# Kernel optimization log

Hardware: AMD Instinct MI355X
Metric: run time of the kernel (lower is better)

## Reference

```python
import jax, jax.numpy as jnp
import numpy as np
from jax import lax

NUM_DISP = 64
BLOCK = 21
EPS = 1e-12  # F.normalize default eps


def _box_sum(v):
    # v: (N, H, W) -> BLOCK x BLOCK zero-padded box sum (same shape), separable.
    p = BLOCK // 2
    v = v[:, None]  # (N,1,H,W)
    kv = jnp.ones((1, 1, BLOCK, 1), v.dtype)
    kh = jnp.ones((1, 1, 1, BLOCK), v.dtype)
    v = lax.conv_general_dilated(v, kv, (1, 1), ((p, p), (0, 0)))
    v = lax.conv_general_dilated(v, kh, (1, 1), ((0, 0), (p, p)))
    return v[:, 0]


def _l2norm_c(img):
    n = jnp.sqrt(jnp.sum(img * img, axis=1, keepdims=True))
    return img / jnp.maximum(n, EPS)


def _disparity(left, right):
    # left, right: (B, 3, H, W)
    left = _l2norm_c(left)
    right = _l2norm_c(right)
    B, C, H, W = left.shape
    d = jnp.arange(NUM_DISP)
    xs = jnp.arange(W)
    idx = xs[None, :] - d[:, None]              # (D, W): source column in right image
    valid = (idx >= 0)
    r_shift = right[:, :, :, jnp.clip(idx, 0)]  # (B, C, H, D, W)
    r_shift = jnp.where(valid[None, None, None], r_shift, 0.0)
    # per-pixel channel-summed absolute difference -> (B, D, H, W)
    diff = jnp.sum(jnp.abs(left[:, :, :, None, :] - r_shift), axis=1)  # (B, H, D, W)
    diff = jnp.transpose(diff, (0, 2, 1, 3))    # (B, D, H, W)
    cost = _box_sum(diff.reshape(B * NUM_DISP, H, W)).reshape(B, NUM_DISP, H, W)
    cost = cost / (C * BLOCK * BLOCK)           # mean SAD over block elements
    return jnp.argmin(cost, axis=1).astype(left.dtype)  # (B, H, W)


def setup_inputs() -> dict:
    key = jax.random.key(0)
    k1, k2 = jax.random.split(key)
    x = jax.random.normal(k1, (2, 6, 320, 512), dtype=jnp.float32)
    gt = jax.random.normal(k2, (2, 6, 320, 512), dtype=jnp.float32)
    return {"x": x, "gt": gt}


def reference(x, gt):
    disp_gt = _disparity(gt[:, :3], gt[:, 3:])
    disp_pred = _disparity(x[:, :3], x[:, 3:])
    return jnp.mean(jnp.abs(disp_pred - disp_gt))
```

## Files before the change

kernel.cpp:

```cpp
#include <hip/hip_runtime.h>
#include <math.h>

constexpr int B = 2, H = 320, W = 512, D = 64;
constexpr int HW = H * W;
constexpr int R = 10;
constexpr int SEG = 80;
constexpr int NSEG = H / SEG;
constexpr float EPS = 1e-12f;
constexpr int PADW = W + 2 * R;

__global__ void k_norm(const float* __restrict__ x, const float* __restrict__ gt,
                       float4* __restrict__ nrm4) {
    int idx = blockIdx.x * blockDim.x + threadIdx.x;
    if (idx >= 2 * B * HW) return;
    int t = idx / (B * HW);
    int rem = idx - t * (B * HW);
    int b = rem / HW;
    int hw = rem - b * HW;
    const float* p = (t == 0 ? x : gt) + (size_t)b * 6 * HW + hw;
    float v0 = p[0],      v1 = p[HW],     v2 = p[2 * HW];
    float v3 = p[3 * HW], v4 = p[4 * HW], v5 = p[5 * HW];
    float n1 = fmaxf(sqrtf(v0 * v0 + v1 * v1 + v2 * v2), EPS);
    float n2 = fmaxf(sqrtf(v3 * v3 + v4 * v4 + v5 * v5), EPS);
    float4* q = nrm4 + (size_t)(t * B + b) * 2 * HW + hw;
    q[0]  = make_float4(v0 / n1, v1 / n1, v2 / n1, 0.f);
    q[HW] = make_float4(v3 / n2, v4 / n2, v5 / n2, 0.f);
}

__global__ void k_cost(const float4* __restrict__ nrm4, float* __restrict__ cost, int t) {
    int blk = blockIdx.x;
    int combo = blk & (2 * NSEG - 1);
    int d = blk >> 3;
    int b = combo >> 2;
    int seg = combo & (NSEG - 1);
    int w = threadIdx.x;
    const float4* L4 = nrm4 + (size_t)(t * B + b) * 2 * HW;
    const float4* R4 = L4 + HW;
    const bool val = (w >= d);
    const int wr = val ? (w - d) : 0;
    const int h0 = seg * SEG;

    __shared__ float srow[2][PADW];
    if (w < R) {
        srow[0][w] = 0.f; srow[1][w] = 0.f;
        srow[0][W + R + w] = 0.f; srow[1][W + R + w] = 0.f;
    }

    auto diff = [&](int h) -> float {
        float4 l = L4[(size_t)h * W + w];
        if (val) {
            float4 r = R4[(size_t)h * W + wr];
            return fabsf(l.x - r.x) + fabsf(l.y - r.y) + fabsf(l.z - r.z);
        }
        return fabsf(l.x) + fabsf(l.y) + fabsf(l.z);
    };

    float ring[2 * R + 1];
    float s = 0.f;
#pragma unroll
    for (int j = 0; j < 2 * R + 1; ++j) {
        int hh = h0 - R + j;
        float v = (hh >= 0 && hh < H) ? diff(hh) : 0.f;
        ring[j] = v;
        s += v;
    }

    float* cp = cost + ((size_t)(b * D + d) * H) * W + w;
    for (int i = 0; i < SEG; ++i) {
        int h = h0 + i;
        float* row = srow[i & 1];
        row[R + w] = s;
        __syncthreads();
        float c = 0.f;
#pragma unroll
        for (int k = 0; k <= 2 * R; ++k) c += row[w + k];
        cp[(size_t)h * W] = c;
        int ha = h + R + 1;
        float nv = (ha < H) ? diff(ha) : 0.f;
        s += nv - ring[0];
#pragma unroll
        for (int j = 0; j < 2 * R; ++j) ring[j] = ring[j + 1];
        ring[2 * R] = nv;
    }
}

__global__ void k_argmin(const float* __restrict__ cost, float* __restrict__ disp) {
    int idx = blockIdx.x * blockDim.x + threadIdx.x;
    if (idx >= B * HW) return;
    int b = idx / HW;
    int hw = idx - b * HW;
    const float* cp = cost + (size_t)b * D * HW + hw;
    float best = 3.4e38f;
    int bd = 0;
    for (int d = 0; d < D; ++d) {
        float v = cp[(size_t)d * HW];
        if (v < best) { best = v; bd = d; }
    }
    disp[idx] = (float)bd;
}

__global__ void k_red1(const float* __restrict__ a, const float* __restrict__ b2,
                       float* __restrict__ part, int n) {
    __shared__ float sm[256];
    int tid = threadIdx.x;
    float s = 0.f;
    for (int i = blockIdx.x * 256 + tid; i < n; i += gridDim.x * 256)
        s += fabsf(a[i] - b2[i]);
    sm[tid] = s;
    __syncthreads();
    for (int off = 128; off; off >>= 1) {
        if (tid < off) sm[tid] += sm[tid + off];
        __syncthreads();
    }
    if (!tid) part[blockIdx.x] = sm[0];
}

__global__ void k_red2(const float* __restrict__ part, float* __restrict__ out,
                       int nb, float inv) {
    __shared__ float sm[256];
    int tid = threadIdx.x;
    float s = 0.f;
    for (int i = tid; i < nb; i += 256) s += part[i];
    sm[tid] = s;
    __syncthreads();
    for (int off = 128; off; off >>= 1) {
        if (tid < off) sm[tid] += sm[tid + off];
        __syncthreads();
    }
    if (!tid) out[0] = sm[0] * inv;
}

extern "C" void kernel_launch(void* const* d_in, const int* in_sizes, int n_in,
                              void* d_out, int out_size, void* d_ws, size_t ws_size,
                              hipStream_t stream) {
    const float* x  = (const float*)d_in[0];
    const float* gt = (const float*)d_in[1];

    float4* nrm4 = (float4*)d_ws;
    float* cost  = (float*)(nrm4 + (size_t)2 * B * 2 * HW);
    float* disp  = cost + (size_t)B * D * HW;
    float* part  = disp + (size_t)2 * B * HW;

    k_norm<<<(2 * B * HW + 255) / 256, 256, 0, stream>>>(x, gt, nrm4);

    for (int t = 0; t < 2; ++t) {
        k_cost<<<B * NSEG * D, W, 0, stream>>>(nrm4, cost, t);
        k_argmin<<<(B * HW + 255) / 256, 256, 0, stream>>>(cost, disp + (size_t)t * B * HW);
    }

    constexpr int NB = 640;
    k_red1<<<NB, 256, 0, stream>>>(disp, disp + (size_t)B * HW, part, B * HW);
    k_red2<<<1, 256, 0, stream>>>(part, (float*)d_out, NB, 1.f / (float)(B * HW));
}
```

Baseline: 241.5 us.

## Batch eight rows per barrier in cost kernel with shared ring and vectorized sliding sums

The cost kernel moves the vertical ring buffer into shared memory and accumulates eight rows of vertical sums before each barrier. Each thread then computes eight horizontal box sums with a running sliding window and writes them as float4 stores. This replaces the per-row barrier and 21 shared reads per output. The argmin kernel now processes four pixels per thread with float4 loads. In exchange the kernel uses more shared memory (about 60 KB per block), which may limit occupancy, and it adds a launch bound.

```diff
diff --git a/kernel.cpp b/kernel.cpp
--- a/kernel.cpp
+++ b/kernel.cpp
@@ -6,8 +6,8 @@
 constexpr int R = 10;
 constexpr int SEG = 80;
 constexpr int NSEG = H / SEG;
+constexpr int RS = 540;
 constexpr float EPS = 1e-12f;
-constexpr int PADW = W + 2 * R;
 
 __global__ void k_norm(const float* __restrict__ x, const float* __restrict__ gt,
                        float4* __restrict__ nrm4) {
@@ -27,12 +27,13 @@
     q[HW] = make_float4(v3 / n2, v4 / n2, v5 / n2, 0.f);
 }
 
-__global__ void k_cost(const float4* __restrict__ nrm4, float* __restrict__ cost, int t) {
+__global__ __launch_bounds__(512, 4) void k_cost(const float4* __restrict__ nrm4,
+                                                 float* __restrict__ cost, int t) {
     int blk = blockIdx.x;
-    int combo = blk & (2 * NSEG - 1);
+    int combo = blk & 7;
     int d = blk >> 3;
     int b = combo >> 2;
-    int seg = combo & (NSEG - 1);
+    int seg = combo & 3;
     int w = threadIdx.x;
     const float4* L4 = nrm4 + (size_t)(t * B + b) * 2 * HW;
     const float4* R4 = L4 + HW;
@@ -40,10 +41,13 @@
     const int wr = val ? (w - d) : 0;
     const int h0 = seg * SEG;
 
-    __shared__ float srow[2][PADW];
-    if (w < R) {
-        srow[0][w] = 0.f; srow[1][w] = 0.f;
-        srow[0][W + R + w] = 0.f; srow[1][W + R + w] = 0.f;
+    __shared__ float ring[21][W];
+    __shared__ float vsbuf[8][RS];
+
+    {
+        int j = w >> 6, k = w & 63;
+        if (k < 10) vsbuf[j][k] = 0.f;
+        else if (k < 28) vsbuf[j][522 + (k - 10)] = 0.f;
     }
 
     auto diff = [&](int h) -> float {
@@ -55,48 +59,74 @@
         return fabsf(l.x) + fabsf(l.y) + fabsf(l.z);
     };
 
-    float ring[2 * R + 1];
-    float s = 0.f;
+    float vs = 0.f;
+    for (int k = 0; k < 20; ++k) {
+        int h = h0 - R + k;
+        float dv = (h >= 0) ? diff(h) : 0.f;
+        ring[k][w] = dv;
+        vs += dv;
+    }
+    ring[20][w] = 0.f;
+
+    float* cp = cost + ((size_t)(b * D + d) * H) * W;
+    const int cc = threadIdx.x >> 3;
+    const int jj = threadIdx.x & 7;
+
+    for (int ss = 0; ss < SEG / 8; ++ss) {
 #pragma unroll
-    for (int j = 0; j < 2 * R + 1; ++j) {
-        int hh = h0 - R + j;
-        float v = (hh >= 0 && hh < H) ? diff(hh) : 0.f;
-        ring[j] = v;
-        s += v;
-    }
-
-    float* cp = cost + ((size_t)(b * D + d) * H) * W + w;
-    for (int i = 0; i < SEG; ++i) {
-        int h = h0 + i;
-        float* row = srow[i & 1];
-        row[R + w] = s;
+        for (int j = 0; j < 8; ++j) {
+            int i = ss * 8 + j;
+            int slot = (i + 20) % 21;
+            int hn = h0 + i + R;
+            float dv = (hn < H) ? diff(hn) : 0.f;
+            float dold = ring[slot][w];
+            ring[slot][w] = dv;
+            vs += dv - dold;
+            vsbuf[j][10 + w] = vs;
+        }
         __syncthreads();
-        float c = 0.f;
+        {
+            const float* vp = &vsbuf[jj][8 * cc];
+            float wnd[28];
 #pragma unroll
-        for (int k = 0; k <= 2 * R; ++k) c += row[w + k];
-        cp[(size_t)h * W] = c;
-        int ha = h + R + 1;
-        float nv = (ha < H) ? diff(ha) : 0.f;
-        s += nv - ring[0];
+            for (int q = 0; q < 7; ++q) {
+                float4 v4 = *(const float4*)(vp + 4 * q);
+                wnd[4 * q] = v4.x; wnd[4 * q + 1] = v4.y;
+                wnd[4 * q + 2] = v4.z; wnd[4 * q + 3] = v4.w;
+            }
+            float o = 0.f;
 #pragma unroll
-        for (int j = 0; j < 2 * R; ++j) ring[j] = ring[j + 1];
-        ring[2 * R] = nv;
+            for (int k = 0; k < 21; ++k) o += wnd[k];
+            float out[8];
+            out[0] = o;
+#pragma unroll
+            for (int k = 1; k < 8; ++k) { o += wnd[20 + k] - wnd[k - 1]; out[k] = o; }
+            float* op = cp + (size_t)(h0 + ss * 8 + jj) * W + 8 * cc;
+            *(float4*)(op)     = make_float4(out[0], out[1], out[2], out[3]);
+            *(float4*)(op + 4) = make_float4(out[4], out[5], out[6], out[7]);
+        }
+        __syncthreads();
     }
 }
 
 __global__ void k_argmin(const float* __restrict__ cost, float* __restrict__ disp) {
-    int idx = blockIdx.x * blockDim.x + threadIdx.x;
-    if (idx >= B * HW) return;
-    int b = idx / HW;
-    int hw = idx - b * HW;
-    const float* cp = cost + (size_t)b * D * HW + hw;
-    float best = 3.4e38f;
-    int bd = 0;
-    for (int d = 0; d < D; ++d) {
-        float v = cp[(size_t)d * HW];
-        if (v < best) { best = v; bd = d; }
+    int idx = blockIdx.x * 256 + threadIdx.x;
+    if (idx >= B * (HW / 4)) return;
+    int b = idx / (HW / 4);
+    int g = idx - b * (HW / 4);
+    const float4* cp = (const float4*)cost + (size_t)b * D * (HW / 4) + g;
+    float4 v0 = cp[0];
+    float bb[4] = {v0.x, v0.y, v0.z, v0.w};
+    int bd[4] = {0, 0, 0, 0};
+#pragma unroll 4
+    for (int d = 1; d < D; ++d) {
+        float4 v = cp[(size_t)d * (HW / 4)];
+        if (v.x < bb[0]) { bb[0] = v.x; bd[0] = d; }
+        if (v.y < bb[1]) { bb[1] = v.y; bd[1] = d; }
+        if (v.z < bb[2]) { bb[2] = v.z; bd[2] = d; }
+        if (v.w < bb[3]) { bb[3] = v.w; bd[3] = d; }
     }
-    disp[idx] = (float)bd;
+    ((float4*)disp)[idx] = make_float4((float)bd[0], (float)bd[1], (float)bd[2], (float)bd[3]);
 }
 
 __global__ void k_red1(const float* __restrict__ a, const float* __restrict__ b2,
@@ -144,8 +174,8 @@
     k_norm<<<(2 * B * HW + 255) / 256, 256, 0, stream>>>(x, gt, nrm4);
 
     for (int t = 0; t < 2; ++t) {
-        k_cost<<<B * NSEG * D, W, 0, stream>>>(nrm4, cost, t);
-        k_argmin<<<(B * HW + 255) / 256, 256, 0, stream>>>(cost, disp + (size_t)t * B * HW);
+        k_cost<<<B * NSEG * D, 512, 0, stream>>>(nrm4, cost, t);
+        k_argmin<<<(B * (HW / 4) + 255) / 256, 256, 0, stream>>>(cost, disp + (size_t)t * B * HW);
     }
 
     constexpr int NB = 640;
```

After: 203.9 us. 1.18x faster.

## Split box filter into vertical-sum pass and fused horizontal-sum argmin kernel

Applied to the files above, without the earlier changes.

The cost kernel now only computes vertical running sums and writes them to a zero-padded row buffer, with no shared memory and no per-row barrier. A new kernel reads those padded rows, applies the horizontal 21-wide sliding sum in registers, and takes the argmin over disparities in the same pass, so the full cost volume is never written and re-read. The second image's pass also folds the absolute-difference loss and a per-block reduction into the argmin kernel, removing the separate reduction kernel. In exchange the vertical-sum buffer is padded and slightly larger, and the normalisation runs per image instead of once for both.

```diff
diff --git a/kernel.cpp b/kernel.cpp
--- a/kernel.cpp
+++ b/kernel.cpp
@@ -4,115 +4,144 @@
 constexpr int B = 2, H = 320, W = 512, D = 64;
 constexpr int HW = H * W;
 constexpr int R = 10;
-constexpr int SEG = 80;
-constexpr int NSEG = H / SEG;
+constexpr int SEG = 80, NSEG = 4;
+constexpr int VS = 536;
 constexpr float EPS = 1e-12f;
-constexpr int PADW = W + 2 * R;
 
-__global__ void k_norm(const float* __restrict__ x, const float* __restrict__ gt,
-                       float4* __restrict__ nrm4) {
-    int idx = blockIdx.x * blockDim.x + threadIdx.x;
-    if (idx >= 2 * B * HW) return;
-    int t = idx / (B * HW);
-    int rem = idx - t * (B * HW);
-    int b = rem / HW;
-    int hw = rem - b * HW;
-    const float* p = (t == 0 ? x : gt) + (size_t)b * 6 * HW + hw;
+__global__ void k_norm(const float* __restrict__ src, float4* __restrict__ nrm4) {
+    int idx = blockIdx.x * 256 + threadIdx.x;
+    if (idx >= B * HW) return;
+    int b = idx / HW, hw = idx - b * HW;
+    const float* p = src + (size_t)b * 6 * HW + hw;
     float v0 = p[0],      v1 = p[HW],     v2 = p[2 * HW];
     float v3 = p[3 * HW], v4 = p[4 * HW], v5 = p[5 * HW];
     float n1 = fmaxf(sqrtf(v0 * v0 + v1 * v1 + v2 * v2), EPS);
     float n2 = fmaxf(sqrtf(v3 * v3 + v4 * v4 + v5 * v5), EPS);
-    float4* q = nrm4 + (size_t)(t * B + b) * 2 * HW + hw;
+    float4* q = nrm4 + (size_t)b * 2 * HW + hw;
     q[0]  = make_float4(v0 / n1, v1 / n1, v2 / n1, 0.f);
     q[HW] = make_float4(v3 / n2, v4 / n2, v5 / n2, 0.f);
 }
 
-__global__ void k_cost(const float4* __restrict__ nrm4, float* __restrict__ cost, int t) {
+__global__ __launch_bounds__(512) void k_vsum(const float4* __restrict__ nrm4,
+                                              float* __restrict__ vsum) {
     int blk = blockIdx.x;
-    int combo = blk & (2 * NSEG - 1);
-    int d = blk >> 3;
-    int b = combo >> 2;
-    int seg = combo & (NSEG - 1);
+    int combo = blk & 7, d = blk >> 3;
+    int b = combo >> 2, seg = combo & 3;
     int w = threadIdx.x;
-    const float4* L4 = nrm4 + (size_t)(t * B + b) * 2 * HW;
+    const float4* L4 = nrm4 + (size_t)b * 2 * HW;
     const float4* R4 = L4 + HW;
     const bool val = (w >= d);
     const int wr = val ? (w - d) : 0;
     const int h0 = seg * SEG;
 
-    __shared__ float srow[2][PADW];
-    if (w < R) {
-        srow[0][w] = 0.f; srow[1][w] = 0.f;
-        srow[0][W + R + w] = 0.f; srow[1][W + R + w] = 0.f;
-    }
-
     auto diff = [&](int h) -> float {
         float4 l = L4[(size_t)h * W + w];
-        if (val) {
-            float4 r = R4[(size_t)h * W + wr];
-            return fabsf(l.x - r.x) + fabsf(l.y - r.y) + fabsf(l.z - r.z);
-        }
-        return fabsf(l.x) + fabsf(l.y) + fabsf(l.z);
+        float4 r = R4[(size_t)h * W + wr];
+        float a = fabsf(l.x - r.x) + fabsf(l.y - r.y) + fabsf(l.z - r.z);
+        float s = fabsf(l.x) + fabsf(l.y) + fabsf(l.z);
+        return val ? a : s;
     };
 
-    float ring[2 * R + 1];
-    float s = 0.f;
+    float ring[21];
+    float vs = 0.f;
 #pragma unroll
-    for (int j = 0; j < 2 * R + 1; ++j) {
-        int hh = h0 - R + j;
-        float v = (hh >= 0 && hh < H) ? diff(hh) : 0.f;
-        ring[j] = v;
-        s += v;
+    for (int k = 0; k < 20; ++k) {
+        int h = h0 - R + k;
+        float dv = diff(h < 0 ? 0 : h);
+        if (h < 0) dv = 0.f;
+        ring[k] = dv;
+        vs += dv;
     }
+    ring[20] = 0.f;
 
-    float* cp = cost + ((size_t)(b * D + d) * H) * W + w;
+    float* vp = vsum + (size_t)((b * D + d) * H) * VS;
+#pragma unroll
     for (int i = 0; i < SEG; ++i) {
         int h = h0 + i;
-        float* row = srow[i & 1];
-        row[R + w] = s;
-        __syncthreads();
-        float c = 0.f;
-#pragma unroll
-        for (int k = 0; k <= 2 * R; ++k) c += row[w + k];
-        cp[(size_t)h * W] = c;
-        int ha = h + R + 1;
-        float nv = (ha < H) ? diff(ha) : 0.f;
-        s += nv - ring[0];
-#pragma unroll
-        for (int j = 0; j < 2 * R; ++j) ring[j] = ring[j + 1];
-        ring[2 * R] = nv;
+        int slot = (i + 20) % 21;
+        int hn = h + R;
+        float dv = diff(hn < H ? hn : H - 1);
+        if (hn >= H) dv = 0.f;
+        float dold = ring[slot];
+        ring[slot] = dv;
+        vs += dv - dold;
+        float* row = vp + (size_t)h * VS;
+        row[12 + w] = vs;
+        if (w < 12) { row[w] = 0.f; row[524 + w] = 0.f; }
     }
 }
 
-__global__ void k_argmin(const float* __restrict__ cost, float* __restrict__ disp) {
-    int idx = blockIdx.x * blockDim.x + threadIdx.x;
-    if (idx >= B * HW) return;
-    int b = idx / HW;
-    int hw = idx - b * HW;
-    const float* cp = cost + (size_t)b * D * HW + hw;
-    float best = 3.4e38f;
-    int bd = 0;
-    for (int d = 0; d < D; ++d) {
-        float v = cp[(size_t)d * HW];
-        if (v < best) { best = v; bd = d; }
+__global__ __launch_bounds__(512) void k_harg(const float* __restrict__ vsum,
+                                              float* __restrict__ disp,
+                                              const float* __restrict__ disp0,
+                                              float* __restrict__ part) {
+    int blk = blockIdx.x;
+    int combo = blk & 7, hh = blk >> 3;
+    int b = combo >> 2, seg = combo & 3;
+    int h = seg * SEG + hh;
+    int dd = threadIdx.x >> 6;
+    int cc = threadIdx.x & 63;
+
+    __shared__ float sv[8][64][8];
+    __shared__ int   sd[8][64][8];
+
+    const float* rowb = vsum + ((size_t)(b * D) * H + h) * VS;
+    float best[8]; int bestd[8];
+#pragma unroll
+    for (int k2 = 0; k2 < 8; ++k2) {
+        int d = dd + 8 * k2;
+        const float4* rp = (const float4*)(rowb + (size_t)d * H * VS) + 2 * cc;
+        float wnd[32];
+#pragma unroll
+        for (int q = 0; q < 8; ++q) {
+            float4 v = rp[q];
+            wnd[4 * q] = v.x; wnd[4 * q + 1] = v.y;
+            wnd[4 * q + 2] = v.z; wnd[4 * q + 3] = v.w;
+        }
+        float o = 0.f;
+#pragma unroll
+        for (int j = 2; j <= 22; ++j) o += wnd[j];
+        float c[8];
+        c[0] = o;
+#pragma unroll
+        for (int k = 1; k < 8; ++k) { o += wnd[k + 22] - wnd[k + 1]; c[k] = o; }
+        if (k2 == 0) {
+#pragma unroll
+            for (int j = 0; j < 8; ++j) { best[j] = c[j]; bestd[j] = d; }
+        } else {
+#pragma unroll
+            for (int j = 0; j < 8; ++j)
+                if (c[j] < best[j]) { best[j] = c[j]; bestd[j] = d; }
+        }
     }
-    disp[idx] = (float)bd;
-}
+#pragma unroll
+    for (int j = 0; j < 8; ++j) { sv[dd][cc][j] = best[j]; sd[dd][cc][j] = bestd[j]; }
+    __syncthreads();
 
-__global__ void k_red1(const float* __restrict__ a, const float* __restrict__ b2,
-                       float* __restrict__ part, int n) {
-    __shared__ float sm[256];
-    int tid = threadIdx.x;
-    float s = 0.f;
-    for (int i = blockIdx.x * 256 + tid; i < n; i += gridDim.x * 256)
-        s += fabsf(a[i] - b2[i]);
-    sm[tid] = s;
-    __syncthreads();
-    for (int off = 128; off; off >>= 1) {
-        if (tid < off) sm[tid] += sm[tid + off];
+    int col = threadIdx.x;
+    int c6 = col >> 3, c7 = col & 7;
+    float bv = sv[0][c6][c7]; int bd = sd[0][c6][c7];
+#pragma unroll
+    for (int q = 1; q < 8; ++q) {
+        float v = sv[q][c6][c7]; int dq = sd[q][c6][c7];
+        if (v < bv || (v == bv && dq < bd)) { bv = v; bd = dq; }
+    }
+    float dres = (float)bd;
+    size_t oidx = (size_t)(b * H + h) * W + col;
+    if (disp0 == nullptr) {
+        disp[oidx] = dres;
+    } else {
+        float ls = fabsf(dres - disp0[oidx]);
         __syncthreads();
+        float* sm = &sv[0][0][0];
+        sm[col] = ls;
+        __syncthreads();
+        for (int off = 256; off; off >>= 1) {
+            if (col < off) sm[col] += sm[col + off];
+            __syncthreads();
+        }
+        if (!col) part[blk] = sm[0];
     }
-    if (!tid) part[blockIdx.x] = sm[0];
 }
 
 __global__ void k_red2(const float* __restrict__ part, float* __restrict__ out,
@@ -137,18 +166,19 @@
     const float* gt = (const float*)d_in[1];
 
     float4* nrm4 = (float4*)d_ws;
-    float* cost  = (float*)(nrm4 + (size_t)2 * B * 2 * HW);
-    float* disp  = cost + (size_t)B * D * HW;
-    float* part  = disp + (size_t)2 * B * HW;
+    float* vsum  = (float*)(nrm4 + (size_t)B * 2 * HW);
+    float* disp0 = vsum + (size_t)B * D * H * VS;
+    float* part  = disp0 + (size_t)B * HW;
 
-    k_norm<<<(2 * B * HW + 255) / 256, 256, 0, stream>>>(x, gt, nrm4);
+    constexpr int NRM_BLKS = (B * HW + 255) / 256;
 
-    for (int t = 0; t < 2; ++t) {
-        k_cost<<<B * NSEG * D, W, 0, stream>>>(nrm4, cost, t);
-        k_argmin<<<(B * HW + 255) / 256, 256, 0, stream>>>(cost, disp + (size_t)t * B * HW);
-    }
+    k_norm<<<NRM_BLKS, 256, 0, stream>>>(x, nrm4);
+    k_vsum<<<B * NSEG * D, 512, 0, stream>>>(nrm4, vsum);
+    k_harg<<<8 * SEG, 512, 0, stream>>>(vsum, disp0, nullptr, nullptr);
 
-    constexpr int NB = 640;
-    k_red1<<<NB, 256, 0, stream>>>(disp, disp + (size_t)B * HW, part, B * HW);
-    k_red2<<<1, 256, 0, stream>>>(part, (float*)d_out, NB, 1.f / (float)(B * HW));
+    k_norm<<<NRM_BLKS, 256, 0, stream>>>(gt, nrm4);
+    k_vsum<<<B * NSEG * D, 512, 0, stream>>>(nrm4, vsum);
+    k_harg<<<8 * SEG, 512, 0, stream>>>(vsum, nullptr, disp0, part);
+
+    k_red2<<<1, 256, 0, stream>>>(part, (float*)d_out, 8 * SEG, 1.f / (float)(B * HW));
 }
```

After: 239.0 us. Within noise of the previous version (-1.1%).
